# Performance work log

Hardware: AMD Instinct MI355X
Metric: run time of the kernel (lower is better)

Reference implementation:

```python
import jax, jax.numpy as jnp
import numpy as np

N = 50000        # nodes
E = 800000       # edges (avg degree 16)
D_IN = 128
HID = 128
K = 3


def cheb_edge_weights(row, col, n):
    # PyG ChebConv sym normalization with assumed lambda_max = 2.0:
    # L_hat = (2/lambda_max) * (I - D^-1/2 A D^-1/2) - I = -D^-1/2 A D^-1/2 (zero diagonal)
    mask = (row != col).astype(jnp.float32)  # remove_self_loops
    deg = jax.ops.segment_sum(mask, row, num_segments=n)
    dinv = jnp.where(deg > 0.0, jax.lax.rsqrt(jnp.maximum(deg, 1.0)), 0.0)
    return -dinv[row] * dinv[col] * mask  # [E]


def cheb_conv(x, row, col, w_edge, W, b, n):
    # Chebyshev recursion: Tx0=x, Tx1=L_hat x, Tx_k = 2 L_hat Tx_{k-1} - Tx_{k-2}
    def prop(h):  # sparse L_hat @ h via gather + segment_sum
        return jax.ops.segment_sum(w_edge[:, None] * h[col], row, num_segments=n)

    Tx0 = x
    out = Tx0 @ W[0]
    Tx1 = prop(Tx0)
    out = out + Tx1 @ W[1]
    for k in range(2, W.shape[0]):
        Tx2 = 2.0 * prop(Tx1) - Tx0
        out = out + Tx2 @ W[k]
        Tx0, Tx1 = Tx1, Tx2
    return out + b


def setup_inputs() -> dict:
    key = jax.random.key(0)
    ks = jax.random.split(key, 8)
    x = jax.random.normal(ks[0], (N, D_IN), dtype=jnp.float32)
    ei = jax.random.randint(ks[1], (2, E), 0, N, dtype=jnp.int32)
    s = 0.05
    W1 = jax.random.normal(ks[2], (K, D_IN, HID), dtype=jnp.float32) * s
    b1 = jnp.zeros((HID,), dtype=jnp.float32)
    W2 = jax.random.normal(ks[3], (K, HID, HID), dtype=jnp.float32) * s
    b2 = jnp.zeros((HID,), dtype=jnp.float32)
    W3 = jax.random.normal(ks[4], (K, HID, HID), dtype=jnp.float32) * s
    b3 = jnp.zeros((HID,), dtype=jnp.float32)
    return {"x": x, "ei": ei, "W1": W1, "b1": b1, "W2": W2, "b2": b2, "W3": W3, "b3": b3}


def reference(x, ei, W1, b1, W2, b2, W3, b3):
    row, col = ei[0], ei[1]
    w_edge = cheb_edge_weights(row, col, N)
    # layer chain: ChebConv -> ReLU -> dropout (eval mode: identity)
    h = jax.nn.relu(cheb_conv(x, row, col, w_edge, W1, b1, N))
    h = jax.nn.relu(cheb_conv(h, row, col, w_edge, W2, b2, N))
    h = jax.nn.relu(cheb_conv(h, row, col, w_edge, W3, b3, N))
    return h
```

## Files before the change

### kernel.cpp

```cpp
#include <hip/hip_runtime.h>
#include <hip/hip_bf16.h>

#define DFEAT 128

typedef short bf16x8 __attribute__((ext_vector_type(8)));
typedef float f32x4  __attribute__((ext_vector_type(4)));
typedef unsigned short u16x8 __attribute__((ext_vector_type(8)));

__device__ __forceinline__ unsigned bf16r(float f) {
    unsigned u = __float_as_uint(f);
    u += 0x7fffu + ((u >> 16) & 1u);
    return u >> 16;
}
__device__ __forceinline__ unsigned pack_bf16(float lo, float hi) {
    return bf16r(lo) | (bf16r(hi) << 16);
}

__global__ void deg_kernel(const int* __restrict__ ei, int* __restrict__ deg8, int E, int N) {
    int e = blockIdx.x * blockDim.x + threadIdx.x;
    if (e < E) {
        int r = ei[e];
        int c = ei[E + e];
        if (r != c) atomicAdd(&deg8[(blockIdx.x & 7) * N + r], 1);
    }
}

__global__ __launch_bounds__(1024) void scan1_kernel(const int* __restrict__ deg8,
                                                     int* __restrict__ poff,
                                                     int* __restrict__ row_ptr,
                                                     int* __restrict__ bsum,
                                                     float* __restrict__ dinv, int n) {
    __shared__ int wsums[16];
    int t = threadIdx.x;
    int idx = blockIdx.x * 1024 + t;
    int tot = 0;
    if (idx < n) {
        int run = 0;
        #pragma unroll
        for (int p = 0; p < 8; ++p) {
            int d = deg8[p * n + idx];
            poff[p * n + idx] = run;
            run += d;
        }
        tot = run;
        dinv[idx] = (tot > 0) ? rsqrtf((float)tot) : 0.f;
    }
    int vi = tot;
    #pragma unroll
    for (int off = 1; off < 64; off <<= 1) {
        int x = __shfl_up(vi, off);
        if ((t & 63) >= off) vi += x;
    }
    if ((t & 63) == 63) wsums[t >> 6] = vi;
    __syncthreads();
    if (t < 16) {
        int s = wsums[t];
        int si = s;
        #pragma unroll
        for (int off = 1; off < 16; off <<= 1) {
            int x = __shfl_up(si, off);
            if (t >= off) si += x;
        }
        wsums[t] = si - s;
        if (t == 15) bsum[blockIdx.x] = si;
    }
    __syncthreads();
    if (idx < n) row_ptr[idx + 1] = wsums[t >> 6] + vi;
}

__global__ void scan2_kernel(int* __restrict__ bsum, int nb) {
    int t = threadIdx.x;
    int carry = 0;
    for (int base = 0; base < nb; base += 64) {
        int v = (base + t < nb) ? bsum[base + t] : 0;
        int vi = v;
        #pragma unroll
        for (int off = 1; off < 64; off <<= 1) {
            int x = __shfl_up(vi, off);
            if (t >= off) vi += x;
        }
        if (base + t < nb) bsum[base + t] = carry + vi - v;
        carry += __shfl(vi, 63);
    }
}

__global__ __launch_bounds__(1024) void scan3_kernel(int* __restrict__ row_ptr,
                                                     const int* __restrict__ bsum, int n) {
    int idx = blockIdx.x * 1024 + threadIdx.x;
    if (idx == 0) row_ptr[0] = 0;
    if (idx < n) row_ptr[idx + 1] += bsum[blockIdx.x];
}

__global__ void fill_kernel(const int* __restrict__ ei, const int* __restrict__ row_ptr,
                            const int* __restrict__ poff, int* __restrict__ fillc8,
                            const float* __restrict__ dinv,
                            unsigned* __restrict__ e_cw, int E, int N) {
    int e = blockIdx.x * blockDim.x + threadIdx.x;
    if (e < E) {
        int r = ei[e];
        int c = ei[E + e];
        if (r != c) {
            int p = blockIdx.x & 7;
            int k = atomicAdd(&fillc8[p * N + r], 1);
            int pos = row_ptr[r] + poff[p * N + r] + k;
            float w = -dinv[r] * dinv[c];
            _Float16 hf = (_Float16)w;
            unsigned short wb;
            __builtin_memcpy(&wb, &hf, 2);
            e_cw[pos] = (unsigned)c | ((unsigned)wb << 16);
        }
    }
}

__global__ void conv_kernel(const float2* __restrict__ x, unsigned* __restrict__ xb, int npk,
                            const float* __restrict__ W1, const float* __restrict__ W2,
                            const float* __restrict__ W3, unsigned short* __restrict__ Wt) {
    int id = blockIdx.x * blockDim.x + threadIdx.x;
    if (id < npk) {
        float2 v = x[id];
        xb[id] = pack_bf16(v.x, v.y);
        return;
    }
    int id2 = id - npk;
    const int PER = 3 * DFEAT * DFEAT;
    if (id2 < 3 * PER) {
        int layer = id2 / PER;
        int rem = id2 - layer * PER;
        const float* W = (layer == 0) ? W1 : ((layer == 1) ? W2 : W3);
        int seg = rem >> 14;
        int k   = (rem >> 7) & 127;
        int nn  = rem & 127;
        Wt[layer * PER + (seg << 14) + (nn << 7) + k] = (unsigned short)bf16r(W[rem]);
    }
}

__global__ __launch_bounds__(256) void prop_bf16_kernel(
    const unsigned* __restrict__ hin, const unsigned* __restrict__ sub,
    unsigned* __restrict__ hout,
    const int* __restrict__ row_ptr, const unsigned* __restrict__ e_cw,
    float alpha, int n)
{
    int wv = __builtin_amdgcn_readfirstlane(threadIdx.x >> 6);
    int node = blockIdx.x * 4 + wv;
    int t = threadIdx.x & 63;
    if (node >= n) return;
    int s = row_ptr[node];
    int e = row_ptr[node + 1];
    float a0 = 0.f, a1 = 0.f;
    int j = s;
    for (; j + 16 <= e; j += 16) {
        unsigned cw[16];
        #pragma unroll
        for (int q = 0; q < 16; ++q) cw[q] = e_cw[j + q];
        unsigned v[16];
        #pragma unroll
        for (int q = 0; q < 16; ++q)
            v[q] = hin[(size_t)(cw[q] & 0xffffu) * 64 + t];
        #pragma unroll
        for (int q = 0; q < 16; ++q) {
            unsigned short wb = (unsigned short)(cw[q] >> 16);
            _Float16 hf; __builtin_memcpy(&hf, &wb, 2);
            float w = (float)hf;
            a0 += w * __uint_as_float(v[q] << 16);
            a1 += w * __uint_as_float(v[q] & 0xffff0000u);
        }
    }
    for (; j + 4 <= e; j += 4) {
        unsigned cw[4];
        #pragma unroll
        for (int q = 0; q < 4; ++q) cw[q] = e_cw[j + q];
        unsigned v[4];
        #pragma unroll
        for (int q = 0; q < 4; ++q)
            v[q] = hin[(size_t)(cw[q] & 0xffffu) * 64 + t];
        #pragma unroll
        for (int q = 0; q < 4; ++q) {
            unsigned short wb = (unsigned short)(cw[q] >> 16);
            _Float16 hf; __builtin_memcpy(&hf, &wb, 2);
            float w = (float)hf;
            a0 += w * __uint_as_float(v[q] << 16);
            a1 += w * __uint_as_float(v[q] & 0xffff0000u);
        }
    }
    for (; j < e; ++j) {
        unsigned cwv = e_cw[j];
        unsigned short wb = (unsigned short)(cwv >> 16);
        _Float16 hf; __builtin_memcpy(&hf, &wb, 2);
        float w = (float)hf;
        unsigned v = hin[(size_t)(cwv & 0xffffu) * 64 + t];
        a0 += w * __uint_as_float(v << 16);
        a1 += w * __uint_as_float(v & 0xffff0000u);
    }
    a0 *= alpha; a1 *= alpha;
    if (sub) {
        unsigned v = sub[(size_t)node * 64 + t];
        a0 -= __uint_as_float(v << 16);
        a1 -= __uint_as_float(v & 0xffff0000u);
    }
    hout[(size_t)node * 64 + t] = pack_bf16(a0, a1);
}

#define WPAD 136
__global__ __launch_bounds__(256) void gemm3_mfma_kernel(
    const unsigned short* __restrict__ X0, const unsigned short* __restrict__ X1,
    const unsigned short* __restrict__ X2,
    const unsigned short* __restrict__ Wt, const float* __restrict__ bias,
    void* __restrict__ out, int n, int out_bf16)
{
    __shared__ unsigned short Ws[DFEAT * WPAD];
    const int t    = threadIdx.x;
    const int wave = t >> 6;
    const int lane = t & 63;
    const int quad = lane >> 4;
    const int l16  = lane & 15;

    const int row_base = blockIdx.x * 128 + wave * 32;
    int r0 = row_base + l16;       if (r0 >= n) r0 = n - 1;
    int r1 = row_base + 16 + l16;  if (r1 >= n) r1 = n - 1;

    const unsigned short* Xps[3] = {X0, X1, X2};

    f32x4 acc[2][8];
    #pragma unroll
    for (int tt = 0; tt < 2; ++tt)
        #pragma unroll
        for (int c = 0; c < 8; ++c) acc[tt][c] = (f32x4){0.f, 0.f, 0.f, 0.f};

    const int srow = t >> 1;
    const int shalf = (t & 1) * 64;

    #pragma unroll
    for (int seg = 0; seg < 3; ++seg) {
        __syncthreads();
        const unsigned short* Wp = Wt + (seg << 14);
        #pragma unroll
        for (int i = 0; i < 8; ++i) {
            *(u16x8*)&Ws[srow * WPAD + shalf + i * 8] =
                *(const u16x8*)&Wp[srow * DFEAT + shalf + i * 8];
        }
        __syncthreads();
        const unsigned short* A0 = Xps[seg] + (size_t)r0 * DFEAT;
        const unsigned short* A1 = Xps[seg] + (size_t)r1 * DFEAT;
        #pragma unroll
        for (int kk = 0; kk < 4; ++kk) {
            const int ko = kk * 32 + quad * 8;
            bf16x8 a0 = *(const bf16x8*)(A0 + ko);
            bf16x8 a1 = *(const bf16x8*)(A1 + ko);
            #pragma unroll
            for (int c = 0; c < 8; ++c) {
                bf16x8 b = *(const bf16x8*)&Ws[(c * 16 + l16) * WPAD + ko];
                acc[0][c] = __builtin_amdgcn_mfma_f32_16x16x32_bf16(a0, b, acc[0][c], 0, 0, 0);
                acc[1][c] = __builtin_amdgcn_mfma_f32_16x16x32_bf16(a1, b, acc[1][c], 0, 0, 0);
            }
        }
    }

    #pragma unroll
    for (int tt = 0; tt < 2; ++tt) {
        int orow0 = blockIdx.x * 128 + wave * 32 + tt * 16 + quad * 4;
        #pragma unroll
        for (int c = 0; c < 8; ++c) {
            int col = c * 16 + l16;
            float bv = bias[col];
            #pragma unroll
            for (int r = 0; r < 4; ++r) {
                int orow = orow0 + r;
                if (orow < n) {
                    float v = fmaxf(acc[tt][c][r] + bv, 0.f);
                    if (out_bf16)
                        ((unsigned short*)out)[(size_t)orow * DFEAT + col] = (unsigned short)bf16r(v);
                    else
                        ((float*)out)[(size_t)orow * DFEAT + col] = v;
                }
            }
        }
    }
}

extern "C" void kernel_launch(void* const* d_in, const int* in_sizes, int n_in,
                              void* d_out, int out_size, void* d_ws, size_t ws_size,
                              hipStream_t stream) {
    const float* x  = (const float*)d_in[0];
    const int*   ei = (const int*)d_in[1];
    const float* W1 = (const float*)d_in[2];
    const float* b1 = (const float*)d_in[3];
    const float* W2 = (const float*)d_in[4];
    const float* b2 = (const float*)d_in[5];
    const float* W3 = (const float*)d_in[6];
    const float* b3 = (const float*)d_in[7];

    const int N = in_sizes[0] / DFEAT;
    const int E = in_sizes[1] / 2;
    const int NPK = N * (DFEAT / 2);
    const int NB = (N + 1023) / 1024;

    unsigned* xb  = (unsigned*)d_ws;
    unsigned* t1b = xb  + NPK;
    unsigned* t2b = t1b + NPK;
    unsigned* ab  = t2b + NPK;
    unsigned short* wt = (unsigned short*)(ab + NPK);
    int*   deg8    = (int*)(wt + 3 * 3 * DFEAT * DFEAT);
    int*   fillc8  = deg8 + 8 * N;
    int*   poff    = fillc8 + 8 * N;
    int*   row_ptr = poff + 8 * N;
    float* dinv    = (float*)(row_ptr + (N + 1));
    unsigned* e_cw = (unsigned*)(dinv + N);
    int*   bsum    = (int*)(e_cw + E);

    hipMemsetAsync(deg8, 0, sizeof(int) * 16 * N, stream);

    deg_kernel<<<(E + 255) / 256, 256, 0, stream>>>(ei, deg8, E, N);
    scan1_kernel<<<NB, 1024, 0, stream>>>(deg8, poff, row_ptr, bsum, dinv, N);
    scan2_kernel<<<1, 64, 0, stream>>>(bsum, NB);
    scan3_kernel<<<NB, 1024, 0, stream>>>(row_ptr, bsum, N);
    fill_kernel<<<(E + 255) / 256, 256, 0, stream>>>(ei, row_ptr, poff, fillc8, dinv, e_cw, E, N);

    const int WELEM = 3 * DFEAT * DFEAT;
    const int CONVT = NPK + 3 * WELEM;
    conv_kernel<<<(CONVT + 255) / 256, 256, 0, stream>>>(
        (const float2*)x, xb, NPK, W1, W2, W3, wt);

    const float* bl[3] = {b1, b2, b3};
    const unsigned* hin = xb;
    const int prop_grid = (N + 3) / 4;
    const int gemm_grid = (N + 127) / 128;
    for (int l = 0; l < 3; ++l) {
        prop_bf16_kernel<<<prop_grid, 256, 0, stream>>>(hin, nullptr, t1b, row_ptr, e_cw, 1.f, N);
        prop_bf16_kernel<<<prop_grid, 256, 0, stream>>>(t1b, hin, t2b, row_ptr, e_cw, 2.f, N);
        void* hout = (l == 2) ? d_out : (void*)ab;
        gemm3_mfma_kernel<<<gemm_grid, 256, 0, stream>>>(
            (const unsigned short*)hin, (const unsigned short*)t1b, (const unsigned short*)t2b,
            wt + l * WELEM, bl[l], hout, N, (l == 2) ? 0 : 1);
        hin = ab;
    }
}
```

Baseline: 404.9 us.

## Fuse graph preprocessing and conversions into one cooperative kernel with grid syncs

Replaces the memset, degree count, three-stage scan, CSR fill and bf16 conversion kernels with a single cooperative persistent kernel that separates the phases with grid-wide syncs. It is meant to remove per-kernel launch gaps and the tail idle time between small kernels. The scan chunk size drops to 256 threads to match the block size. In exchange it adds several grid barriers and grid-stride loops over a fixed 1024-block grid, which must fit co-resident on the device.

```diff
diff --git a/kernel.cpp b/kernel.cpp
--- a/kernel.cpp
+++ b/kernel.cpp
@@ -1,5 +1,6 @@
 #include <hip/hip_runtime.h>
 #include <hip/hip_bf16.h>
+#include <hip/hip_cooperative_groups.h>
 
 #define DFEAT 128
 
@@ -16,87 +17,105 @@
     return bf16r(lo) | (bf16r(hi) << 16);
 }
 
-__global__ void deg_kernel(const int* __restrict__ ei, int* __restrict__ deg8, int E, int N) {
-    int e = blockIdx.x * blockDim.x + threadIdx.x;
-    if (e < E) {
+__global__ __launch_bounds__(256) void prep_kernel(
+    const int* __restrict__ ei, int E, int N,
+    int* __restrict__ deg8, int* __restrict__ fillc8, int* __restrict__ poff,
+    int* __restrict__ row_ptr, int* __restrict__ bsum,
+    float* __restrict__ dinv, unsigned* __restrict__ e_cw,
+    const float2* __restrict__ x, unsigned* __restrict__ xb, int npk,
+    const float* __restrict__ W1, const float* __restrict__ W2,
+    const float* __restrict__ W3, unsigned short* __restrict__ Wt)
+{
+    cooperative_groups::grid_group grid = cooperative_groups::this_grid();
+    const int t = threadIdx.x;
+    const int gid = blockIdx.x * 256 + t;
+    const int gstride = gridDim.x * 256;
+
+    for (int i = gid; i < 16 * N; i += gstride) deg8[i] = 0;
+    for (int i = gid; i < npk; i += gstride) {
+        float2 v = x[i];
+        xb[i] = pack_bf16(v.x, v.y);
+    }
+    const int PER = 3 * DFEAT * DFEAT;
+    for (int i = gid; i < 3 * PER; i += gstride) {
+        int layer = i / PER;
+        int rem = i - layer * PER;
+        const float* W = (layer == 0) ? W1 : ((layer == 1) ? W2 : W3);
+        int seg = rem >> 14, k = (rem >> 7) & 127, nn = rem & 127;
+        Wt[layer * PER + (seg << 14) + (nn << 7) + k] = (unsigned short)bf16r(W[rem]);
+    }
+    grid.sync();
+
+    for (int e = gid; e < E; e += gstride) {
         int r = ei[e];
         int c = ei[E + e];
         if (r != c) atomicAdd(&deg8[(blockIdx.x & 7) * N + r], 1);
     }
-}
-
-__global__ __launch_bounds__(1024) void scan1_kernel(const int* __restrict__ deg8,
-                                                     int* __restrict__ poff,
-                                                     int* __restrict__ row_ptr,
-                                                     int* __restrict__ bsum,
-                                                     float* __restrict__ dinv, int n) {
-    __shared__ int wsums[16];
-    int t = threadIdx.x;
-    int idx = blockIdx.x * 1024 + t;
-    int tot = 0;
-    if (idx < n) {
-        int run = 0;
-        #pragma unroll
-        for (int p = 0; p < 8; ++p) {
-            int d = deg8[p * n + idx];
-            poff[p * n + idx] = run;
-            run += d;
-        }
-        tot = run;
-        dinv[idx] = (tot > 0) ? rsqrtf((float)tot) : 0.f;
-    }
-    int vi = tot;
-    #pragma unroll
-    for (int off = 1; off < 64; off <<= 1) {
-        int x = __shfl_up(vi, off);
-        if ((t & 63) >= off) vi += x;
-    }
-    if ((t & 63) == 63) wsums[t >> 6] = vi;
-    __syncthreads();
-    if (t < 16) {
-        int s = wsums[t];
-        int si = s;
-        #pragma unroll
-        for (int off = 1; off < 16; off <<= 1) {
-            int x = __shfl_up(si, off);
-            if (t >= off) si += x;
-        }
-        wsums[t] = si - s;
-        if (t == 15) bsum[blockIdx.x] = si;
-    }
-    __syncthreads();
-    if (idx < n) row_ptr[idx + 1] = wsums[t >> 6] + vi;
-}
-
-__global__ void scan2_kernel(int* __restrict__ bsum, int nb) {
-    int t = threadIdx.x;
-    int carry = 0;
-    for (int base = 0; base < nb; base += 64) {
-        int v = (base + t < nb) ? bsum[base + t] : 0;
-        int vi = v;
+    grid.sync();
+
+    __shared__ int wsums[4];
+    const int NCH = (N + 255) >> 8;
+    for (int ch = blockIdx.x; ch < NCH; ch += gridDim.x) {
+        int idx = ch * 256 + t;
+        int tot = 0;
+        if (idx < N) {
+            int run = 0;
+            #pragma unroll
+            for (int p = 0; p < 8; ++p) {
+                int d = deg8[p * N + idx];
+                poff[p * N + idx] = run;
+                run += d;
+            }
+            tot = run;
+            dinv[idx] = (tot > 0) ? rsqrtf((float)tot) : 0.f;
+        }
+        int vi = tot;
         #pragma unroll
         for (int off = 1; off < 64; off <<= 1) {
-            int x = __shfl_up(vi, off);
-            if (t >= off) vi += x;
-        }
-        if (base + t < nb) bsum[base + t] = carry + vi - v;
-        carry += __shfl(vi, 63);
-    }
-}
-
-__global__ __launch_bounds__(1024) void scan3_kernel(int* __restrict__ row_ptr,
-                                                     const int* __restrict__ bsum, int n) {
-    int idx = blockIdx.x * 1024 + threadIdx.x;
-    if (idx == 0) row_ptr[0] = 0;
-    if (idx < n) row_ptr[idx + 1] += bsum[blockIdx.x];
-}
-
-__global__ void fill_kernel(const int* __restrict__ ei, const int* __restrict__ row_ptr,
-                            const int* __restrict__ poff, int* __restrict__ fillc8,
-                            const float* __restrict__ dinv,
-                            unsigned* __restrict__ e_cw, int E, int N) {
-    int e = blockIdx.x * blockDim.x + threadIdx.x;
-    if (e < E) {
+            int xs = __shfl_up(vi, off);
+            if ((t & 63) >= off) vi += xs;
+        }
+        if ((t & 63) == 63) wsums[t >> 6] = vi;
+        __syncthreads();
+        if (t < 4) {
+            int s = wsums[t];
+            int si = s;
+            #pragma unroll
+            for (int off = 1; off < 4; off <<= 1) {
+                int xs = __shfl_up(si, off);
+                if (t >= off) si += xs;
+            }
+            wsums[t] = si - s;
+            if (t == 3) bsum[ch] = si;
+        }
+        __syncthreads();
+        if (idx < N) row_ptr[idx + 1] = wsums[t >> 6] + vi;
+        __syncthreads();
+    }
+    grid.sync();
+
+    if (blockIdx.x == 0 && t < 64) {
+        int carry = 0;
+        for (int base = 0; base < NCH; base += 64) {
+            int v = (base + t < NCH) ? bsum[base + t] : 0;
+            int vi = v;
+            #pragma unroll
+            for (int off = 1; off < 64; off <<= 1) {
+                int xs = __shfl_up(vi, off);
+                if (t >= off) vi += xs;
+            }
+            if (base + t < NCH) bsum[base + t] = carry + vi - v;
+            carry += __shfl(vi, 63);
+        }
+    }
+    grid.sync();
+
+    if (gid == 0) row_ptr[0] = 0;
+    for (int idx = gid; idx < N; idx += gstride)
+        row_ptr[idx + 1] += bsum[idx >> 8];
+    grid.sync();
+
+    for (int e = gid; e < E; e += gstride) {
         int r = ei[e];
         int c = ei[E + e];
         if (r != c) {
@@ -109,28 +128,6 @@
             __builtin_memcpy(&wb, &hf, 2);
             e_cw[pos] = (unsigned)c | ((unsigned)wb << 16);
         }
-    }
-}
-
-__global__ void conv_kernel(const float2* __restrict__ x, unsigned* __restrict__ xb, int npk,
-                            const float* __restrict__ W1, const float* __restrict__ W2,
-                            const float* __restrict__ W3, unsigned short* __restrict__ Wt) {
-    int id = blockIdx.x * blockDim.x + threadIdx.x;
-    if (id < npk) {
-        float2 v = x[id];
-        xb[id] = pack_bf16(v.x, v.y);
-        return;
-    }
-    int id2 = id - npk;
-    const int PER = 3 * DFEAT * DFEAT;
-    if (id2 < 3 * PER) {
-        int layer = id2 / PER;
-        int rem = id2 - layer * PER;
-        const float* W = (layer == 0) ? W1 : ((layer == 1) ? W2 : W3);
-        int seg = rem >> 14;
-        int k   = (rem >> 7) & 127;
-        int nn  = rem & 127;
-        Wt[layer * PER + (seg << 14) + (nn << 7) + k] = (unsigned short)bf16r(W[rem]);
     }
 }
 
@@ -292,7 +289,7 @@
     const int N = in_sizes[0] / DFEAT;
     const int E = in_sizes[1] / 2;
     const int NPK = N * (DFEAT / 2);
-    const int NB = (N + 1023) / 1024;
+    const int NCH = (N + 255) / 256;
 
     unsigned* xb  = (unsigned*)d_ws;
     unsigned* t1b = xb  + NPK;
@@ -307,23 +304,26 @@
     unsigned* e_cw = (unsigned*)(dinv + N);
     int*   bsum    = (int*)(e_cw + E);
 
-    hipMemsetAsync(deg8, 0, sizeof(int) * 16 * N, stream);
-
-    deg_kernel<<<(E + 255) / 256, 256, 0, stream>>>(ei, deg8, E, N);
-    scan1_kernel<<<NB, 1024, 0, stream>>>(deg8, poff, row_ptr, bsum, dinv, N);
-    scan2_kernel<<<1, 64, 0, stream>>>(bsum, NB);
-    scan3_kernel<<<NB, 1024, 0, stream>>>(row_ptr, bsum, N);
-    fill_kernel<<<(E + 255) / 256, 256, 0, stream>>>(ei, row_ptr, poff, fillc8, dinv, e_cw, E, N);
-
-    const int WELEM = 3 * DFEAT * DFEAT;
-    const int CONVT = NPK + 3 * WELEM;
-    conv_kernel<<<(CONVT + 255) / 256, 256, 0, stream>>>(
-        (const float2*)x, xb, NPK, W1, W2, W3, wt);
+    {
+        const float2* x2 = (const float2*)x;
+        const int* eip = ei;
+        int Ev = E, Nv = N, npkv = NPK;
+        void* args[] = {
+            (void*)&eip, (void*)&Ev, (void*)&Nv,
+            (void*)&deg8, (void*)&fillc8, (void*)&poff, (void*)&row_ptr, (void*)&bsum,
+            (void*)&dinv, (void*)&e_cw,
+            (void*)&x2, (void*)&xb, (void*)&npkv,
+            (void*)&W1, (void*)&W2, (void*)&W3, (void*)&wt
+        };
+        hipLaunchCooperativeKernel((void*)prep_kernel, dim3(1024), dim3(256),
+                                   args, 0, stream);
+    }
 
     const float* bl[3] = {b1, b2, b3};
     const unsigned* hin = xb;
     const int prop_grid = (N + 3) / 4;
     const int gemm_grid = (N + 127) / 128;
+    const int WELEM = 3 * DFEAT * DFEAT;
     for (int l = 0; l < 3; ++l) {
         prop_bf16_kernel<<<prop_grid, 256, 0, stream>>>(hin, nullptr, t1b, row_ptr, e_cw, 1.f, N);
         prop_bf16_kernel<<<prop_grid, 256, 0, stream>>>(t1b, hin, t2b, row_ptr, e_cw, 2.f, N);
```

New measurement: 915.2 us. 2.26x slower.
